# Optimization experiments

Hardware: AMD Instinct MI355X
Metric: run time of the kernel (lower is better)

Reference implementation:

```python
import jax, jax.numpy as jnp
import numpy as np

DIM = 16
FDIM = 16
KNN = 10
N = 1_000_000


def setup_inputs() -> dict:
    key = jax.random.key(0)
    k1, k2, k3, k4, k5, k6 = jax.random.split(key, 6)
    xknn = jax.random.normal(k1, (N, DIM, KNN), dtype=jnp.float32)
    x = jax.random.normal(k2, (N, DIM), dtype=jnp.float32)
    # mlpF = Conv1d(dim, F, 1): weight [F, dim] (kernel size 1 squeezed), bias [F]
    s = 1.0 / np.sqrt(DIM)
    Wf = jax.random.normal(k3, (FDIM, DIM), dtype=jnp.float32) * s
    bf = jax.random.normal(k4, (FDIM,), dtype=jnp.float32) * s
    # mlp1 = Conv1d(F, 1, 1): weight [F], bias scalar
    s1 = 1.0 / np.sqrt(FDIM)
    W1 = jax.random.normal(k5, (FDIM,), dtype=jnp.float32) * s1
    b1 = jax.random.normal(k6, (), dtype=jnp.float32) * s1
    return {"xknn": xknn, "x": x, "Wf": Wf, "bf": bf, "W1": W1, "b1": b1}


def reference(xknn, x, Wf, bf, W1, b1):
    n = xknn.shape[0]
    x2 = xknn.reshape(n, DIM, KNN)                       # [N, dim, K]
    # mlpF on neighbors: Conv1d(dim->F, k=1)
    h2 = jnp.einsum('fd,ndk->nfk', Wf, x2) + bf[:, None]  # [N, F, K]
    a2 = jnp.einsum('f,nfk->nk', W1, h2)[:, None, :] + b1  # mlp1 -> [N, 1, K]
    # mlpF + mlp1 on center point
    x1 = x.reshape(n, DIM, 1)
    h1 = jnp.einsum('fd,ndk->nfk', Wf, x1) + bf[:, None]   # [N, F, 1]
    a1 = jnp.einsum('f,nfk->nk', W1, h1) + b1              # [N, 1] (squeeze+unsqueeze)
    # per-slice additive attention logits (the python loop in the original)
    logits = a2 + a1[:, :, None]                           # [N, 1, K]
    # torch Fn.softmax with implicit dim on 3D tensor -> dim=0 (faithful)
    xc = jax.nn.softmax(logits, axis=0)                    # [N, 1, K]
    # values: mlpF(x2) again, then a raw reshape [N,F,K]->[N,K,F] (not transpose)
    x2v = h2.reshape(n, KNN, FDIM)                         # [N, K, F]
    x_attn = jnp.matmul(xc, x2v)                           # [N, 1, F]
    return x_attn.squeeze(), x2v
```

## Files before the change

kernel.cpp:

```cpp
#include <hip/hip_runtime.h>
#include <math.h>


#define TPTS 32
#define ROWF 164

__device__ __forceinline__ void comb(float& m, float& s, float om, float os) {
  float M = fmaxf(m, om);
  if (M == -INFINITY) return;
  s = s * __expf(m - M) + os * __expf(om - M);
  m = M;
}

template <int CTRL>
__device__ __forceinline__ float dppmov(float v) {
  return __int_as_float(__builtin_amdgcn_update_dpp(
      0, __float_as_int(v), CTRL, 0xf, 0xf, true));
}

__device__ __forceinline__ float sum16(float v) {
  v += dppmov<0xB1>(v);
  v += dppmov<0x4E>(v);
  v += dppmov<0x141>(v);
  v += dppmov<0x140>(v);
  return v;
}

__device__ __forceinline__ float f4e(const float4& v, int e) {
  return (e == 0) ? v.x : (e == 1) ? v.y : (e == 2) ? v.z : v.w;
}

__global__ __launch_bounds__(256) void gap_k1(
    const float* __restrict__ xknn, const float* __restrict__ x,
    const float* __restrict__ Wf, const float* __restrict__ bf,
    const float* __restrict__ W1, const float* __restrict__ b1p,
    float* __restrict__ out, float* __restrict__ partials, int n) {
  __shared__ float sm[TPTS * ROWF];
  __shared__ float s_red[4][10][2];

  const int tid = threadIdx.x;
  const int lane = tid & 63;
  const int wave = tid >> 6;
  const int f = lane & 15;
  const int g = tid >> 4;

  float wfo[16];
#pragma unroll
  for (int dq = 0; dq < 4; ++dq) {
    float4 v = *(const float4*)(Wf + f * 16 + 4 * dq);
    wfo[4 * dq + 0] = v.x;
    wfo[4 * dq + 1] = v.y;
    wfo[4 * dq + 2] = v.z;
    wfo[4 * dq + 3] = v.w;
  }
  const float w1o = W1[f];
  const float bfo = bf[f];
  float u_own = 0.f;
#pragma unroll
  for (int j = 0; j < 16; ++j) u_own = fmaf(W1[j], Wf[j * 16 + f], u_own);
  const float addA = 2.0f * b1p[0];

  float rm = -INFINITY, rs = 0.f;

  float* out0 = out;
  float* out1 = out + (size_t)n * 16;

  const long ntiles = (long)n / TPTS;

  for (long t = (long)blockIdx.x; t < ntiles; t += gridDim.x) {
    const unsigned base = (unsigned)t * TPTS;
    __syncthreads();

    {
      const float* src = xknn + (size_t)base * 160;
#pragma unroll
      for (int i = 0; i < 5; ++i) {
        const int F4 = tid + 256 * i;
        const float4 v = *(const float4*)(src + 4 * F4);
        const int p = F4 / 40;
        const int s4 = F4 - p * 40;
        *(float4*)(&sm[p * ROWF + 4 * s4]) = v;
      }
    }
    __syncthreads();

#pragma unroll
    for (int rep = 0; rep < 2; ++rep) {
      const int pl = g + 16 * rep;
      const unsigned pt = base + (unsigned)pl;
      const float* sp = &sm[pl * ROWF];
      const float xo = x[(size_t)pt * 16 + f];

      float acc[10];
#pragma unroll
      for (int k = 0; k < 10; ++k) acc[k] = bfo;
#pragma unroll
      for (int J = 0; J < 40; ++J) {
        const float4 v = *(const float4*)(sp + 4 * J);
#pragma unroll
        for (int e = 0; e < 4; ++e) {
          const int r = 4 * J + e, d = r / 10, k = r - d * 10;
          acc[k] = fmaf(wfo[d], f4e(v, e), acc[k]);
        }
      }

      float* o1 = out1 + ((size_t)pt * 160 + 10 * f);
      *(float2*)(o1 + 0) = make_float2(acc[0], acc[1]);
      *(float2*)(o1 + 2) = make_float2(acc[2], acc[3]);
      *(float2*)(o1 + 4) = make_float2(acc[4], acc[5]);
      *(float2*)(o1 + 6) = make_float2(acc[6], acc[7]);
      *(float2*)(o1 + 8) = make_float2(acc[8], acc[9]);

      float lj = 0.f;
#pragma unroll
      for (int k = 0; k < 10; ++k) {
        const float s = sum16(w1o * acc[k]);
        lj = (k == f) ? s : lj;
      }
      lj += sum16(u_own * xo) + addA;

      if (f < 10) {
        out0[(size_t)pt * 16 + f] = lj;
        const float M = fmaxf(rm, lj);
        rs = rs * __expf(rm - M) + __expf(lj - M);
        rm = M;
      }
    }
  }

  {
    float om = __shfl_xor(rm, 16), os = __shfl_xor(rs, 16);
    comb(rm, rs, om, os);
    om = __shfl_xor(rm, 32); os = __shfl_xor(rs, 32);
    comb(rm, rs, om, os);
  }
  if (lane < 10) {
    s_red[wave][lane][0] = rm;
    s_red[wave][lane][1] = rs;
  }
  __syncthreads();
  if (tid < 10) {
    float m = s_red[0][tid][0], s = s_red[0][tid][1];
    comb(m, s, s_red[1][tid][0], s_red[1][tid][1]);
    comb(m, s, s_red[2][tid][0], s_red[2][tid][1]);
    comb(m, s, s_red[3][tid][0], s_red[3][tid][1]);
    partials[(size_t)blockIdx.x * 20 + tid * 2 + 0] = m;
    partials[(size_t)blockIdx.x * 20 + tid * 2 + 1] = s;
  }
}

__global__ __launch_bounds__(256) void gap_k2(const float* __restrict__ part,
                                              int nb, float* __restrict__ fin) {
  const int k = blockIdx.x;
  const int tid = threadIdx.x;
  float m = -INFINITY, s = 0.f;
  for (int i = tid; i < nb; i += 256)
    comb(m, s, part[(size_t)i * 20 + k * 2], part[(size_t)i * 20 + k * 2 + 1]);
#pragma unroll
  for (int mask = 1; mask < 64; mask <<= 1) {
    float om = __shfl_xor(m, mask, 64);
    float os = __shfl_xor(s, mask, 64);
    comb(m, s, om, os);
  }
  __shared__ float sm[4][2];
  const int wave = tid >> 6, lane = tid & 63;
  if (lane == 0) { sm[wave][0] = m; sm[wave][1] = s; }
  __syncthreads();
  if (tid == 0) {
    for (int w = 1; w < 4; ++w) comb(m, s, sm[w][0], sm[w][1]);
    fin[k * 2 + 0] = m;
    fin[k * 2 + 1] = s;
  }
}

__global__ __launch_bounds__(256) void gap_k3(const float* __restrict__ fin,
                                              float* __restrict__ out, int n) {
  __shared__ float s_fin[20];
  if (threadIdx.x < 20) s_fin[threadIdx.x] = fin[threadIdx.x];
  __syncthreads();
  float mk[10], rsk[10];
#pragma unroll
  for (int k = 0; k < 10; ++k) {
    mk[k] = s_fin[2 * k];
    rsk[k] = 1.0f / s_fin[2 * k + 1];
  }
  float* out0 = out;
  const float* out1 = out + (size_t)n * 16;
  const int q = threadIdx.x & 3;
  const int pl = threadIdx.x >> 2;
  for (long i = (long)blockIdx.x * 64 + pl; i < n; i += (long)gridDim.x * 64) {
    float* lrow = out0 + i * 16;
    float4 la = *(const float4*)(lrow);
    float4 lb = *(const float4*)(lrow + 4);
    float2 lc = *(const float2*)(lrow + 8);
    float l[10] = {la.x, la.y, la.z, la.w, lb.x, lb.y, lb.z, lb.w, lc.x, lc.y};
    float w[10];
#pragma unroll
    for (int k = 0; k < 10; ++k) w[k] = __expf(l[k] - mk[k]) * rsk[k];
    const float* vrow = out1 + i * 160 + q * 4;
    float4 acc = make_float4(0.f, 0.f, 0.f, 0.f);
#pragma unroll
    for (int k = 0; k < 10; ++k) {
      float4 v = *(const float4*)(vrow + k * 16);
      float wk = w[k];
      acc.x = fmaf(wk, v.x, acc.x);
      acc.y = fmaf(wk, v.y, acc.y);
      acc.z = fmaf(wk, v.z, acc.z);
      acc.w = fmaf(wk, v.w, acc.w);
    }
    *(float4*)(lrow + q * 4) = acc;
  }
}

extern "C" void kernel_launch(void* const* d_in, const int* in_sizes, int n_in,
                              void* d_out, int out_size, void* d_ws, size_t ws_size,
                              hipStream_t stream) {
  const float* xknn = (const float*)d_in[0];
  const float* x    = (const float*)d_in[1];
  const float* Wf   = (const float*)d_in[2];
  const float* bf   = (const float*)d_in[3];
  const float* W1   = (const float*)d_in[4];
  const float* b1   = (const float*)d_in[5];
  float* out = (float*)d_out;
  const int n = in_sizes[1] / 16;

  const int G1 = 1792;
  float* partials = (float*)d_ws;
  float* finals = partials + (size_t)G1 * 20;

  gap_k1<<<G1, 256, 0, stream>>>(xknn, x, Wf, bf, W1, b1, out, partials, n);
  gap_k2<<<10, 256, 0, stream>>>(partials, G1, finals);
  gap_k3<<<2048, 256, 0, stream>>>(finals, out, n);
}
```

Before: 500.5 us.

## Double-buffer neighbor tiles in LDS with register prefetch of next tile

Switches the main kernel to a double-buffered shared-memory pipeline. The next tile's xknn data is loaded into registers before the current tile is computed, and is written into the alternate LDS buffer afterwards, leaving one barrier per iteration. The tile shrinks from 32 to 16 points, so each thread handles one point per iteration instead of two. The aim is to hide global load latency behind compute, at the cost of more registers and twice as many loop iterations and barriers.

```diff
diff --git a/kernel.cpp b/kernel.cpp
--- a/kernel.cpp
+++ b/kernel.cpp
@@ -2,7 +2,7 @@
 #include <math.h>
 
 
-#define TPTS 32
+#define TPTS 16
 #define ROWF 164
 
 __device__ __forceinline__ void comb(float& m, float& s, float om, float os) {
@@ -35,7 +35,7 @@
     const float* __restrict__ Wf, const float* __restrict__ bf,
     const float* __restrict__ W1, const float* __restrict__ b1p,
     float* __restrict__ out, float* __restrict__ partials, int n) {
-  __shared__ float sm[TPTS * ROWF];
+  __shared__ float sm[2][TPTS * ROWF];
   __shared__ float s_red[4][10][2];
 
   const int tid = threadIdx.x;
@@ -43,6 +43,12 @@
   const int wave = tid >> 6;
   const int f = lane & 15;
   const int g = tid >> 4;
+
+  const int F0 = tid, F1 = tid + 256, F2 = tid + 512;
+  const unsigned l0 = (unsigned)((F0 / 40) * ROWF + (F0 % 40) * 4);
+  const unsigned l1 = (unsigned)((F1 / 40) * ROWF + (F1 % 40) * 4);
+  const unsigned l2 = (unsigned)((F2 / 40) * ROWF + (F2 % 40) * 4);
+  const bool has2 = (F2 < TPTS * 40);
 
   float wfo[16];
 #pragma unroll
@@ -66,66 +72,80 @@
   float* out1 = out + (size_t)n * 16;
 
   const long ntiles = (long)n / TPTS;
-
-  for (long t = (long)blockIdx.x; t < ntiles; t += gridDim.x) {
-    const unsigned base = (unsigned)t * TPTS;
+  const long G = gridDim.x;
+  long t = (long)blockIdx.x;
+  int cur = 0;
+
+  float4 st0, st1, st2;
+
+  {
+    const float* src = xknn + (size_t)t * (TPTS * 160);
+    st0 = *(const float4*)(src + 4 * F0);
+    st1 = *(const float4*)(src + 4 * F1);
+    st2 = st0;
+    if (has2) st2 = *(const float4*)(src + 4 * F2);
+    *(float4*)(&sm[0][l0]) = st0;
+    *(float4*)(&sm[0][l1]) = st1;
+    if (has2) *(float4*)(&sm[0][l2]) = st2;
+  }
+
+  for (; t < ntiles; t += G) {
     __syncthreads();
 
-    {
-      const float* src = xknn + (size_t)base * 160;
-#pragma unroll
-      for (int i = 0; i < 5; ++i) {
-        const int F4 = tid + 256 * i;
-        const float4 v = *(const float4*)(src + 4 * F4);
-        const int p = F4 / 40;
-        const int s4 = F4 - p * 40;
-        *(float4*)(&sm[p * ROWF + 4 * s4]) = v;
+    const long tn = t + G;
+    const bool more = (tn < ntiles);
+    if (more) {
+      const float* src = xknn + (size_t)tn * (TPTS * 160);
+      st0 = *(const float4*)(src + 4 * F0);
+      st1 = *(const float4*)(src + 4 * F1);
+      if (has2) st2 = *(const float4*)(src + 4 * F2);
+    }
+
+    const unsigned pt = (unsigned)t * TPTS + (unsigned)g;
+    const float* sp = &sm[cur][g * ROWF];
+    const float xo = x[(size_t)pt * 16 + f];
+
+    float acc[10];
+#pragma unroll
+    for (int k = 0; k < 10; ++k) acc[k] = bfo;
+#pragma unroll
+    for (int J = 0; J < 40; ++J) {
+      const float4 v = *(const float4*)(sp + 4 * J);
+#pragma unroll
+      for (int e = 0; e < 4; ++e) {
+        const int r = 4 * J + e, d = r / 10, k = r - d * 10;
+        acc[k] = fmaf(wfo[d], f4e(v, e), acc[k]);
       }
     }
-    __syncthreads();
-
-#pragma unroll
-    for (int rep = 0; rep < 2; ++rep) {
-      const int pl = g + 16 * rep;
-      const unsigned pt = base + (unsigned)pl;
-      const float* sp = &sm[pl * ROWF];
-      const float xo = x[(size_t)pt * 16 + f];
-
-      float acc[10];
-#pragma unroll
-      for (int k = 0; k < 10; ++k) acc[k] = bfo;
-#pragma unroll
-      for (int J = 0; J < 40; ++J) {
-        const float4 v = *(const float4*)(sp + 4 * J);
-#pragma unroll
-        for (int e = 0; e < 4; ++e) {
-          const int r = 4 * J + e, d = r / 10, k = r - d * 10;
-          acc[k] = fmaf(wfo[d], f4e(v, e), acc[k]);
-        }
-      }
-
-      float* o1 = out1 + ((size_t)pt * 160 + 10 * f);
-      *(float2*)(o1 + 0) = make_float2(acc[0], acc[1]);
-      *(float2*)(o1 + 2) = make_float2(acc[2], acc[3]);
-      *(float2*)(o1 + 4) = make_float2(acc[4], acc[5]);
-      *(float2*)(o1 + 6) = make_float2(acc[6], acc[7]);
-      *(float2*)(o1 + 8) = make_float2(acc[8], acc[9]);
-
-      float lj = 0.f;
-#pragma unroll
-      for (int k = 0; k < 10; ++k) {
-        const float s = sum16(w1o * acc[k]);
-        lj = (k == f) ? s : lj;
-      }
-      lj += sum16(u_own * xo) + addA;
-
-      if (f < 10) {
-        out0[(size_t)pt * 16 + f] = lj;
-        const float M = fmaxf(rm, lj);
-        rs = rs * __expf(rm - M) + __expf(lj - M);
-        rm = M;
-      }
-    }
+
+    float* o1 = out1 + ((size_t)pt * 160 + 10 * f);
+    *(float2*)(o1 + 0) = make_float2(acc[0], acc[1]);
+    *(float2*)(o1 + 2) = make_float2(acc[2], acc[3]);
+    *(float2*)(o1 + 4) = make_float2(acc[4], acc[5]);
+    *(float2*)(o1 + 6) = make_float2(acc[6], acc[7]);
+    *(float2*)(o1 + 8) = make_float2(acc[8], acc[9]);
+
+    float lj = 0.f;
+#pragma unroll
+    for (int k = 0; k < 10; ++k) {
+      const float s = sum16(w1o * acc[k]);
+      lj = (k == f) ? s : lj;
+    }
+    lj += sum16(u_own * xo) + addA;
+
+    if (f < 10) {
+      out0[(size_t)pt * 16 + f] = lj;
+      const float M = fmaxf(rm, lj);
+      rs = rs * __expf(rm - M) + __expf(lj - M);
+      rm = M;
+    }
+
+    if (more) {
+      *(float4*)(&sm[cur ^ 1][l0]) = st0;
+      *(float4*)(&sm[cur ^ 1][l1]) = st1;
+      if (has2) *(float4*)(&sm[cur ^ 1][l2]) = st2;
+    }
+    cur ^= 1;
   }
 
   {
```

Result: no change. 499.7 us (-0.2%).
